# Kernel tuning notes

Hardware: AMD Instinct MI355X
Metric: run time of the kernel (lower is better)

The kernel has to match this reference:

```python
import jax, jax.numpy as jnp
import numpy as np

TEMPERATURE = 8.0  # sqrt(head_dim=64)
NEG_BIG = -10000.0


def setup_inputs() -> dict:
    key = jax.random.key(0)
    kq, kk, kv, km = jax.random.split(key, 4)
    B, H, S, D, K = 4, 8, 1024, 64, 4
    q = jax.random.normal(kq, (B, H, S, D), dtype=jnp.float32)
    k = jax.random.normal(kk, (B, H, S, D), dtype=jnp.float32)
    v = jax.random.normal(kv, (B, H, S, D), dtype=jnp.float32)
    # K binary attention masks, broadcastable to [B,H,S,S]
    mask = jax.random.randint(km, (K, 1, 1, S, S), 0, 2).astype(jnp.float32)
    return {"q": q, "k": k, "v": v, "mask": mask}


def reference(q, k, v, mask):
    # attn: [B,H,S,S]
    attn = jnp.einsum("bhsd,bhtd->bhst", q / TEMPERATURE, k)
    # additive mask: [K,1,1,S,S]
    ext_mask = (1.0 - mask) * NEG_BIG
    # batched over K instead of the original python loop: [K,B,H,S,S]
    probs = jax.nn.softmax(attn[None] + ext_mask, axis=-1)
    # dropout is identity in eval mode (deterministic reference)
    output = jnp.einsum("kbhst,bhtd->kbhsd", probs, v)
    return (output, attn)
```

## Files before the change

kernel.cpp:

```cpp
#include <hip/hip_runtime.h>
#include <hip/hip_bf16.h>
#include <stdint.h>

typedef float f4 __attribute__((ext_vector_type(4)));
typedef short bf8 __attribute__((ext_vector_type(8)));
typedef uint32_t u4 __attribute__((ext_vector_type(4)));
typedef uint32_t u2 __attribute__((ext_vector_type(2)));

#define SDIM 1024
#define DDIM 64
#define NBH  32
#define KM   4
#define NT   16

#define MB_BLK 4096
#define KB_BLK 1024
#define VT_BLK 512

__device__ __forceinline__ unsigned short f2bf(float f) {
  uint32_t u = __builtin_bit_cast(uint32_t, f);
  u += 0x7fffu + ((u >> 16) & 1u);
  return (unsigned short)(u >> 16);
}

#define GLOAD16(gsrc, ldst)                                                  \
  __builtin_amdgcn_global_load_lds(                                          \
      (const __attribute__((address_space(1))) unsigned int*)(gsrc),         \
      (__attribute__((address_space(3))) unsigned int*)(ldst), 16, 0, 0)

__device__ __forceinline__ bf8 lds_ld(const unsigned short* base, int row, int e0) {
  return *(const bf8*)((const char*)base + (((row * 64 + e0) * 2) ^ ((row & 7) << 4)));
}

__global__ __launch_bounds__(256) void prepass(
    const float* __restrict__ k, const float* __restrict__ v,
    const float* __restrict__ mask, unsigned short* __restrict__ kb,
    unsigned short* __restrict__ vt, uint32_t* __restrict__ mb2) {
  __shared__ float tv[64][65];
  const int b = blockIdx.x;
  const int t = threadIdx.x;
  if (b < MB_BLK) {
    int gid4 = (b * 256 + t) * 4;
    f4 x = *(const f4*)(mask + gid4);
    uint32_t bits = (x[0] > 0.5f ? 1u : 0u) | (x[1] > 0.5f ? 2u : 0u) |
                    (x[2] > 0.5f ? 4u : 0u) | (x[3] > 0.5f ? 8u : 0u);
    uint32_t wv = bits << (gid4 & 28);
    wv |= __shfl_xor(wv, 1);
    wv |= __shfl_xor(wv, 2);
    wv |= __shfl_xor(wv, 4);
    if ((t & 7) == 0) {
      int m = gid4 >> 20;
      int r = (gid4 >> 10) & 1023;
      int c = gid4 & 1023;
      mb2[m * 32768 + (c >> 5) * 1024 + r] = wv;
    }
  } else if (b < MB_BLK + KB_BLK) {
    int base = ((b - MB_BLK) * 256 + t) * 8;
    f4 a = *(const f4*)(k + base);
    f4 c = *(const f4*)(k + base + 4);
    bf8 o;
    o[0] = (short)f2bf(a[0]); o[1] = (short)f2bf(a[1]);
    o[2] = (short)f2bf(a[2]); o[3] = (short)f2bf(a[3]);
    o[4] = (short)f2bf(c[0]); o[5] = (short)f2bf(c[1]);
    o[6] = (short)f2bf(c[2]); o[7] = (short)f2bf(c[3]);
    *(bf8*)(kb + base) = o;
  } else {
    int vb = b - MB_BLK - KB_BLK;
    int bh = vb >> 4;
    int s0 = (vb & 15) * 64;
    int sr = t >> 2, c0 = (t & 3) * 16;
    const float* vp = v + ((size_t)(bh * SDIM) + s0 + sr) * DDIM + c0;
#pragma unroll
    for (int i = 0; i < 4; ++i) {
      f4 x = *(const f4*)(vp + 4 * i);
#pragma unroll
      for (int j = 0; j < 4; ++j) tv[sr][c0 + 4 * i + j] = x[j];
    }
    __syncthreads();
    int d = t >> 2, sc0 = (t & 3) * 16;
    unsigned short tmp[16];
#pragma unroll
    for (int i = 0; i < 16; ++i) tmp[i] = f2bf(tv[sc0 + i][d]);
    unsigned short* op = vt + ((size_t)(bh * DDIM) + d) * SDIM + s0 + sc0;
    bf8 o0, o1;
#pragma unroll
    for (int j = 0; j < 8; ++j) { o0[j] = (short)tmp[j]; o1[j] = (short)tmp[j + 8]; }
    *(bf8*)(op) = o0;
    *(bf8*)(op + 8) = o1;
  }
}

__global__ __launch_bounds__(512, 4) void attn_main(
    const float* __restrict__ qf, const unsigned short* __restrict__ kb,
    const unsigned short* __restrict__ vtg, const uint32_t* __restrict__ mb2,
    float* __restrict__ outO, float* __restrict__ attn) {
  __shared__ __align__(16) unsigned short k_s0[64 * 64];
  __shared__ __align__(16) unsigned short k_s1[64 * 64];
  __shared__ __align__(16) unsigned short v_s0[64 * 64];
  __shared__ __align__(16) unsigned short v_s1[64 * 64];
  __shared__ __align__(16) unsigned short e_s[64 * 64];

  const int tid = threadIdx.x;
  const int l   = tid & 63;
  const int w   = tid >> 6;
  const int l16 = l & 15;
  const int lg  = l >> 4;
  const int rt  = w >> 1;
  const int cp  = w & 1;

  int bid = (int)blockIdx.x;
  bid = (bid & 7) * 64 + (bid >> 3);
  const int bh = bid >> 4;
  const int r0 = (bid & 15) * 64;

  const int srow = tid >> 3;
  const int sd   = ((tid & 7) ^ (srow & 7)) << 3;
  const unsigned short* ksrc = kb  + ((size_t)(bh * SDIM) + srow) * DDIM + sd;
  const unsigned short* vsrc = vtg + ((size_t)(bh * DDIM) + srow) * SDIM + sd;

  GLOAD16(ksrc, k_s0 + tid * 8);
  GLOAD16(vsrc, v_s0 + tid * 8);

  bf8 bq0, bq1;
  {
    const float* qp = qf + ((size_t)(bh * SDIM) + r0 + 16 * rt + l16) * DDIM + lg * 8;
    f4 a0 = *(const f4*)qp;
    f4 a1 = *(const f4*)(qp + 4);
    f4 a2 = *(const f4*)(qp + 32);
    f4 a3 = *(const f4*)(qp + 36);
#pragma unroll
    for (int j = 0; j < 4; ++j) {
      bq0[j]     = (short)f2bf(a0[j] * 0.125f);
      bq0[j + 4] = (short)f2bf(a1[j] * 0.125f);
      bq1[j]     = (short)f2bf(a2[j] * 0.125f);
      bq1[j + 4] = (short)f2bf(a3[j] * 0.125f);
    }
  }

  f4 acc[2][4] = {};
  f4 accl[2]   = {};
  bf8 ones;
#pragma unroll
  for (int b = 0; b < 8; ++b) ones[b] = (short)0x3F80;

  const uint32_t* mbase = mb2 + rt * 32768 + r0 + l16;

  uint32_t mdwA[2][2], mdwB[2][2];
#pragma unroll
  for (int mt2 = 0; mt2 < 2; ++mt2)
#pragma unroll
    for (int kt = 0; kt < 2; ++kt)
      mdwA[mt2][kt] = mbase[kt * 1024 + 32 * cp + 16 * mt2];

  __syncthreads();

#define BODY(CT, KR, VR, KW, VW, MR, MW, PF)                                   \
  {                                                                            \
    if (PF) {                                                                  \
      GLOAD16(ksrc + (size_t)((CT) + 1) * 4096, (KW) + tid * 8);               \
      GLOAD16(vsrc + (size_t)((CT) + 1) * 64, (VW) + tid * 8);                 \
    }                                                                          \
    {                                                                          \
      const int kc0 = 32 * cp + l16;                                           \
      bf8 ak0 = lds_ld((KR), kc0, lg * 8);                                     \
      bf8 ak1 = lds_ld((KR), kc0, lg * 8 + 32);                                \
      bf8 ak2 = lds_ld((KR), kc0 + 16, lg * 8);                                \
      bf8 ak3 = lds_ld((KR), kc0 + 16, lg * 8 + 32);                           \
      f4 s0 = {}, s1 = {};                                                     \
      s0 = __builtin_amdgcn_mfma_f32_16x16x32_bf16(ak0, bq0, s0, 0, 0, 0);     \
      s0 = __builtin_amdgcn_mfma_f32_16x16x32_bf16(ak1, bq1, s0, 0, 0, 0);     \
      s1 = __builtin_amdgcn_mfma_f32_16x16x32_bf16(ak2, bq0, s1, 0, 0, 0);     \
      s1 = __builtin_amdgcn_mfma_f32_16x16x32_bf16(ak3, bq1, s1, 0, 0, 0);     \
      float* arow = attn + ((size_t)(bh * SDIM) + r0 + 16 * rt + l16) * SDIM   \
                    + (CT) * 64 + 32 * cp + 4 * lg;                            \
      *(f4*)(arow) = s0;                                                       \
      *(f4*)(arow + 16) = s1;                                                  \
      const int erow = 16 * rt + l16;                                          \
      u2 ev0, ev1;                                                             \
      ev0[0] = (uint32_t)f2bf(__expf(s0[0])) | ((uint32_t)f2bf(__expf(s0[1])) << 16); \
      ev0[1] = (uint32_t)f2bf(__expf(s0[2])) | ((uint32_t)f2bf(__expf(s0[3])) << 16); \
      ev1[0] = (uint32_t)f2bf(__expf(s1[0])) | ((uint32_t)f2bf(__expf(s1[1])) << 16); \
      ev1[1] = (uint32_t)f2bf(__expf(s1[2])) | ((uint32_t)f2bf(__expf(s1[3])) << 16); \
      const int colA = 32 * cp + 4 * lg;                                       \
      *(u2*)((char*)e_s + (((erow * 64 + colA) * 2) ^ ((erow & 7) << 4))) = ev0; \
      *(u2*)((char*)e_s + (((erow * 64 + colA + 16) * 2) ^ ((erow & 7) << 4))) = ev1; \
    }                                                                          \
    asm volatile("s_waitcnt lgkmcnt(0)\n\ts_barrier" ::: "memory");            \
    {                                                                          \
      bf8 af[2][2];                                                            \
      _Pragma("unroll") for (int mt2 = 0; mt2 < 2; ++mt2) {                    \
        const int row = 32 * cp + 16 * mt2 + l16;                              \
        _Pragma("unroll") for (int kt = 0; kt < 2; ++kt) {                     \
          bf8 e = lds_ld(e_s, row, kt * 32 + lg * 8);                          \
          uint32_t bits = ((MR)[mt2][kt] >> (lg * 8)) & 0xffu;                 \
          u4 ew = __builtin_bit_cast(u4, e);                                   \
          _Pragma("unroll") for (int d = 0; d < 4; ++d) {                      \
            uint32_t n2 = (bits >> (2 * d)) & 3u;                              \
            uint32_t sp = (n2 * 0x8001u) & 0x00010001u;                        \
            ew[d] &= (sp << 16) - sp;                                          \
          }                                                                    \
          af[mt2][kt] = __builtin_bit_cast(bf8, ew);                           \
        }                                                                      \
        accl[mt2] = __builtin_amdgcn_mfma_f32_16x16x32_bf16(af[mt2][0], ones, accl[mt2], 0, 0, 0); \
        accl[mt2] = __builtin_amdgcn_mfma_f32_16x16x32_bf16(af[mt2][1], ones, accl[mt2], 0, 0, 0); \
      }                                                                        \
      _Pragma("unroll") for (int nt = 0; nt < 4; ++nt) {                       \
        const int dc = 16 * nt + l16;                                          \
        bf8 bv0 = lds_ld((VR), dc, lg * 8);                                    \
        bf8 bv1 = lds_ld((VR), dc, lg * 8 + 32);                               \
        _Pragma("unroll") for (int mt2 = 0; mt2 < 2; ++mt2) {                  \
          acc[mt2][nt] = __builtin_amdgcn_mfma_f32_16x16x32_bf16(af[mt2][0], bv0, acc[mt2][nt], 0, 0, 0); \
          acc[mt2][nt] = __builtin_amdgcn_mfma_f32_16x16x32_bf16(af[mt2][1], bv1, acc[mt2][nt], 0, 0, 0); \
        }                                                                      \
      }                                                                        \
    }                                                                          \
    if (PF) {                                                                  \
      _Pragma("unroll") for (int mt2 = 0; mt2 < 2; ++mt2)                      \
        _Pragma("unroll") for (int kt = 0; kt < 2; ++kt)                       \
          (MW)[mt2][kt] = mbase[(((CT) + 1) * 2 + kt) * 1024 + 32 * cp + 16 * mt2]; \
    }                                                                          \
    __syncthreads();                                                           \
  }

  for (int ct2 = 0; ct2 < NT / 2; ++ct2) {
    BODY(2 * ct2,     k_s0, v_s0, k_s1, v_s1, mdwA, mdwB, true);
    BODY(2 * ct2 + 1, k_s1, v_s1, k_s0, v_s0, mdwB, mdwA, (ct2 < NT / 2 - 1));
  }
#undef BODY

#pragma unroll
  for (int mt2 = 0; mt2 < 2; ++mt2) {
#pragma unroll
    for (int r = 0; r < 4; ++r) {
      float inv = 1.0f / accl[mt2][r];
      int row = 32 * cp + 16 * mt2 + 4 * lg + r;
      float* orow = outO + (((size_t)(rt * NBH + bh)) * SDIM + r0 + row) * DDIM + l16;
#pragma unroll
      for (int nt = 0; nt < 4; ++nt)
        orow[16 * nt] = acc[mt2][nt][r] * inv;
    }
  }
}

extern "C" void kernel_launch(void* const* d_in, const int* in_sizes, int n_in,
                              void* d_out, int out_size, void* d_ws, size_t ws_size,
                              hipStream_t stream) {
  (void)in_sizes; (void)n_in; (void)out_size; (void)ws_size;
  const float* q    = (const float*)d_in[0];
  const float* k    = (const float*)d_in[1];
  const float* v    = (const float*)d_in[2];
  const float* mask = (const float*)d_in[3];
  float* outO = (float*)d_out;
  float* attn = (float*)d_out + (size_t)KM * NBH * SDIM * DDIM;

  char* ws = (char*)d_ws;
  unsigned short* kb = (unsigned short*)ws;
  unsigned short* vt = (unsigned short*)(ws + (4u << 20));
  uint32_t*       mb = (uint32_t*)(ws + (8u << 20));

  prepass<<<MB_BLK + KB_BLK + VT_BLK, 256, 0, stream>>>(k, v, mask, kb, vt, mb);
  attn_main<<<NBH * 16, 512, 0, stream>>>(q, kb, vt, mb, outO, attn);
}
```

Before: 54.48 us.

## Double key tile width to 128 columns per iteration, halving barrier count

The per-iteration key/value tile grows from 64 to 128 columns, so the loop runs 8 tiles instead of 16 and needs half as many barriers and prefetch rounds. LDS buffers double in size (about 80KB per block), and the e_s and V layouts switch to 128-wide swizzled rows. The mask words per tile grow to match. The larger LDS footprint may cut how many blocks fit per CU under launch_bounds(512,4).

```diff
diff --git a/kernel.cpp b/kernel.cpp
--- a/kernel.cpp
+++ b/kernel.cpp
@@ -11,7 +11,7 @@
 #define DDIM 64
 #define NBH  32
 #define KM   4
-#define NT   16
+#define NT2  8
 
 #define MB_BLK 4096
 #define KB_BLK 1024
@@ -30,6 +30,9 @@
 
 __device__ __forceinline__ bf8 lds_ld(const unsigned short* base, int row, int e0) {
   return *(const bf8*)((const char*)base + (((row * 64 + e0) * 2) ^ ((row & 7) << 4)));
+}
+__device__ __forceinline__ bf8 lds_ld128(const unsigned short* base, int row, int e0) {
+  return *(const bf8*)((const char*)base + (((row * 128 + e0) * 2) ^ ((row & 7) << 4)));
 }
 
 __global__ __launch_bounds__(256) void prepass(
@@ -94,11 +97,11 @@
     const float* __restrict__ qf, const unsigned short* __restrict__ kb,
     const unsigned short* __restrict__ vtg, const uint32_t* __restrict__ mb2,
     float* __restrict__ outO, float* __restrict__ attn) {
-  __shared__ __align__(16) unsigned short k_s0[64 * 64];
-  __shared__ __align__(16) unsigned short k_s1[64 * 64];
-  __shared__ __align__(16) unsigned short v_s0[64 * 64];
-  __shared__ __align__(16) unsigned short v_s1[64 * 64];
-  __shared__ __align__(16) unsigned short e_s[64 * 64];
+  __shared__ __align__(16) unsigned short k_s0[128 * 64];
+  __shared__ __align__(16) unsigned short k_s1[128 * 64];
+  __shared__ __align__(16) unsigned short v_s0[64 * 128];
+  __shared__ __align__(16) unsigned short v_s1[64 * 128];
+  __shared__ __align__(16) unsigned short e_s[64 * 128];
 
   const int tid = threadIdx.x;
   const int l   = tid & 63;
@@ -113,13 +116,18 @@
   const int bh = bid >> 4;
   const int r0 = (bid & 15) * 64;
 
-  const int srow = tid >> 3;
-  const int sd   = ((tid & 7) ^ (srow & 7)) << 3;
-  const unsigned short* ksrc = kb  + ((size_t)(bh * SDIM) + srow) * DDIM + sd;
-  const unsigned short* vsrc = vtg + ((size_t)(bh * DDIM) + srow) * SDIM + sd;
-
-  GLOAD16(ksrc, k_s0 + tid * 8);
-  GLOAD16(vsrc, v_s0 + tid * 8);
+  const int krow = tid >> 3;
+  const int kswz = ((tid & 7) ^ (krow & 7)) << 3;
+  const unsigned short* ksrc = kb + ((size_t)(bh * SDIM) + krow) * DDIM + kswz;
+  const int vrow = tid >> 4;
+  const int vg   = (tid & 8) | ((tid & 7) ^ (vrow & 7));
+  const unsigned short* vsrcA = vtg + ((size_t)(bh * DDIM) + vrow) * SDIM + vg * 8;
+  const unsigned short* vsrcB = vtg + ((size_t)(bh * DDIM) + vrow + 32) * SDIM + vg * 8;
+
+  GLOAD16(ksrc,        k_s0 + tid * 8);
+  GLOAD16(ksrc + 4096, k_s0 + (tid + 512) * 8);
+  GLOAD16(vsrcA, v_s0 + tid * 8);
+  GLOAD16(vsrcB, v_s0 + (tid + 512) * 8);
 
   bf8 bq0, bq1;
   {
@@ -145,11 +153,11 @@
 
   const uint32_t* mbase = mb2 + rt * 32768 + r0 + l16;
 
-  uint32_t mdwA[2][2], mdwB[2][2];
+  uint32_t mdwA[2][4], mdwB[2][4];
 #pragma unroll
   for (int mt2 = 0; mt2 < 2; ++mt2)
 #pragma unroll
-    for (int kt = 0; kt < 2; ++kt)
+    for (int kt = 0; kt < 4; ++kt)
       mdwA[mt2][kt] = mbase[kt * 1024 + 32 * cp + 16 * mt2];
 
   __syncthreads();
@@ -157,41 +165,37 @@
 #define BODY(CT, KR, VR, KW, VW, MR, MW, PF)                                   \
   {                                                                            \
     if (PF) {                                                                  \
-      GLOAD16(ksrc + (size_t)((CT) + 1) * 4096, (KW) + tid * 8);               \
-      GLOAD16(vsrc + (size_t)((CT) + 1) * 64, (VW) + tid * 8);                 \
+      GLOAD16(ksrc + (size_t)((CT) + 1) * 8192,        (KW) + tid * 8);        \
+      GLOAD16(ksrc + (size_t)((CT) + 1) * 8192 + 4096, (KW) + (tid + 512) * 8);\
+      GLOAD16(vsrcA + (size_t)((CT) + 1) * 128, (VW) + tid * 8);               \
+      GLOAD16(vsrcB + (size_t)((CT) + 1) * 128, (VW) + (tid + 512) * 8);       \
     }                                                                          \
     {                                                                          \
-      const int kc0 = 32 * cp + l16;                                           \
-      bf8 ak0 = lds_ld((KR), kc0, lg * 8);                                     \
-      bf8 ak1 = lds_ld((KR), kc0, lg * 8 + 32);                                \
-      bf8 ak2 = lds_ld((KR), kc0 + 16, lg * 8);                                \
-      bf8 ak3 = lds_ld((KR), kc0 + 16, lg * 8 + 32);                           \
-      f4 s0 = {}, s1 = {};                                                     \
-      s0 = __builtin_amdgcn_mfma_f32_16x16x32_bf16(ak0, bq0, s0, 0, 0, 0);     \
-      s0 = __builtin_amdgcn_mfma_f32_16x16x32_bf16(ak1, bq1, s0, 0, 0, 0);     \
-      s1 = __builtin_amdgcn_mfma_f32_16x16x32_bf16(ak2, bq0, s1, 0, 0, 0);     \
-      s1 = __builtin_amdgcn_mfma_f32_16x16x32_bf16(ak3, bq1, s1, 0, 0, 0);     \
-      float* arow = attn + ((size_t)(bh * SDIM) + r0 + 16 * rt + l16) * SDIM   \
-                    + (CT) * 64 + 32 * cp + 4 * lg;                            \
-      *(f4*)(arow) = s0;                                                       \
-      *(f4*)(arow + 16) = s1;                                                  \
       const int erow = 16 * rt + l16;                                          \
-      u2 ev0, ev1;                                                             \
-      ev0[0] = (uint32_t)f2bf(__expf(s0[0])) | ((uint32_t)f2bf(__expf(s0[1])) << 16); \
-      ev0[1] = (uint32_t)f2bf(__expf(s0[2])) | ((uint32_t)f2bf(__expf(s0[3])) << 16); \
-      ev1[0] = (uint32_t)f2bf(__expf(s1[0])) | ((uint32_t)f2bf(__expf(s1[1])) << 16); \
-      ev1[1] = (uint32_t)f2bf(__expf(s1[2])) | ((uint32_t)f2bf(__expf(s1[3])) << 16); \
-      const int colA = 32 * cp + 4 * lg;                                       \
-      *(u2*)((char*)e_s + (((erow * 64 + colA) * 2) ^ ((erow & 7) << 4))) = ev0; \
-      *(u2*)((char*)e_s + (((erow * 64 + colA + 16) * 2) ^ ((erow & 7) << 4))) = ev1; \
+      float* arow = attn + ((size_t)(bh * SDIM) + r0 + erow) * SDIM            \
+                    + (CT) * 128 + 64 * cp + 4 * lg;                           \
+      _Pragma("unroll") for (int j = 0; j < 4; ++j) {                          \
+        const int kc = 64 * cp + 16 * j + l16;                                 \
+        bf8 ak0 = lds_ld((KR), kc, lg * 8);                                    \
+        bf8 ak1 = lds_ld((KR), kc, lg * 8 + 32);                               \
+        f4 sv = {};                                                            \
+        sv = __builtin_amdgcn_mfma_f32_16x16x32_bf16(ak0, bq0, sv, 0, 0, 0);   \
+        sv = __builtin_amdgcn_mfma_f32_16x16x32_bf16(ak1, bq1, sv, 0, 0, 0);   \
+        *(f4*)(arow + 16 * j) = sv;                                            \
+        u2 ev;                                                                 \
+        ev[0] = (uint32_t)f2bf(__expf(sv[0])) | ((uint32_t)f2bf(__expf(sv[1])) << 16); \
+        ev[1] = (uint32_t)f2bf(__expf(sv[2])) | ((uint32_t)f2bf(__expf(sv[3])) << 16); \
+        const int col = 64 * cp + 16 * j + 4 * lg;                             \
+        *(u2*)((char*)e_s + (((erow * 128 + col) * 2) ^ ((erow & 7) << 4))) = ev; \
+      }                                                                        \
     }                                                                          \
     asm volatile("s_waitcnt lgkmcnt(0)\n\ts_barrier" ::: "memory");            \
     {                                                                          \
-      bf8 af[2][2];                                                            \
-      _Pragma("unroll") for (int mt2 = 0; mt2 < 2; ++mt2) {                    \
-        const int row = 32 * cp + 16 * mt2 + l16;                              \
-        _Pragma("unroll") for (int kt = 0; kt < 2; ++kt) {                     \
-          bf8 e = lds_ld(e_s, row, kt * 32 + lg * 8);                          \
+      _Pragma("unroll") for (int kt = 0; kt < 4; ++kt) {                       \
+        bf8 af[2];                                                             \
+        _Pragma("unroll") for (int mt2 = 0; mt2 < 2; ++mt2) {                  \
+          const int row = 32 * cp + 16 * mt2 + l16;                            \
+          bf8 e = lds_ld128(e_s, row, kt * 32 + lg * 8);                       \
           uint32_t bits = ((MR)[mt2][kt] >> (lg * 8)) & 0xffu;                 \
           u4 ew = __builtin_bit_cast(u4, e);                                   \
           _Pragma("unroll") for (int d = 0; d < 4; ++d) {                      \
@@ -199,32 +203,28 @@
             uint32_t sp = (n2 * 0x8001u) & 0x00010001u;                        \
             ew[d] &= (sp << 16) - sp;                                          \
           }                                                                    \
-          af[mt2][kt] = __builtin_bit_cast(bf8, ew);                           \
+          af[mt2] = __builtin_bit_cast(bf8, ew);                               \
+          accl[mt2] = __builtin_amdgcn_mfma_f32_16x16x32_bf16(af[mt2], ones, accl[mt2], 0, 0, 0); \
         }                                                                      \
-        accl[mt2] = __builtin_amdgcn_mfma_f32_16x16x32_bf16(af[mt2][0], ones, accl[mt2], 0, 0, 0); \
-        accl[mt2] = __builtin_amdgcn_mfma_f32_16x16x32_bf16(af[mt2][1], ones, accl[mt2], 0, 0, 0); \
-      }                                                                        \
-      _Pragma("unroll") for (int nt = 0; nt < 4; ++nt) {                       \
-        const int dc = 16 * nt + l16;                                          \
-        bf8 bv0 = lds_ld((VR), dc, lg * 8);                                    \
-        bf8 bv1 = lds_ld((VR), dc, lg * 8 + 32);                               \
-        _Pragma("unroll") for (int mt2 = 0; mt2 < 2; ++mt2) {                  \
-          acc[mt2][nt] = __builtin_amdgcn_mfma_f32_16x16x32_bf16(af[mt2][0], bv0, acc[mt2][nt], 0, 0, 0); \
-          acc[mt2][nt] = __builtin_amdgcn_mfma_f32_16x16x32_bf16(af[mt2][1], bv1, acc[mt2][nt], 0, 0, 0); \
+        _Pragma("unroll") for (int nt = 0; nt < 4; ++nt) {                     \
+          const int dc = 16 * nt + l16;                                        \
+          bf8 bv = lds_ld128((VR), dc, kt * 32 + lg * 8);                      \
+          _Pragma("unroll") for (int mt2 = 0; mt2 < 2; ++mt2)                  \
+            acc[mt2][nt] = __builtin_amdgcn_mfma_f32_16x16x32_bf16(af[mt2], bv, acc[mt2][nt], 0, 0, 0); \
         }                                                                      \
       }                                                                        \
     }                                                                          \
     if (PF) {                                                                  \
       _Pragma("unroll") for (int mt2 = 0; mt2 < 2; ++mt2)                      \
-        _Pragma("unroll") for (int kt = 0; kt < 2; ++kt)                       \
-          (MW)[mt2][kt] = mbase[(((CT) + 1) * 2 + kt) * 1024 + 32 * cp + 16 * mt2]; \
+        _Pragma("unroll") for (int kt = 0; kt < 4; ++kt)                       \
+          (MW)[mt2][kt] = mbase[(((CT) + 1) * 4 + kt) * 1024 + 32 * cp + 16 * mt2]; \
     }                                                                          \
     __syncthreads();                                                           \
   }
 
-  for (int ct2 = 0; ct2 < NT / 2; ++ct2) {
+  for (int ct2 = 0; ct2 < NT2 / 2; ++ct2) {
     BODY(2 * ct2,     k_s0, v_s0, k_s1, v_s1, mdwA, mdwB, true);
-    BODY(2 * ct2 + 1, k_s1, v_s1, k_s0, v_s0, mdwB, mdwA, (ct2 < NT / 2 - 1));
+    BODY(2 * ct2 + 1, k_s1, v_s1, k_s0, v_s0, mdwB, mdwA, (ct2 < NT2 / 2 - 1));
   }
 #undef BODY
 
```

Result: slower. 71.14 us (+30.6%).
